# Kernel tuning notes

Measured on AMD Instinct MI355X. Metric: run time of the kernel, lower is better.

The kernel has to match this reference:

```python
import jax, jax.numpy as jnp
import numpy as np

N, D, E, K = 65536, 2048, 64, 8
EPS = 1e-5


def setup_inputs() -> dict:
    key = jax.random.key(0)
    kx, kw = jax.random.split(key)
    x = jax.random.normal(kx, (N, D), dtype=jnp.float32)
    # nn.Linear(input_size, num_experts, bias=False) weight: [E, D]
    W = jax.random.normal(kw, (E, D), dtype=jnp.float32) * (1.0 / np.sqrt(D))
    return {"x": x, "W": W}


def _l1_normalize(v):
    # torch F.normalize(p=1, dim=0): v / max(||v||_1, 1e-12)
    return v / jnp.maximum(jnp.sum(jnp.abs(v)), 1e-12)


def reference(x, W):
    # router logits: [N, E] in float32 (matches .float() in torch code)
    logits = (x @ W.T).astype(jnp.float32)
    top_v, top_i = jax.lax.top_k(logits, K)            # [N, K]
    top_k_gates = jax.nn.softmax(top_v, axis=-1).astype(x.dtype)
    # training-branch aux loss (compute_aux_loss)
    probs = jax.nn.softmax(logits, axis=-1)            # [N, E]
    rows = jnp.arange(logits.shape[0])[:, None]
    dense_gates = jnp.zeros_like(probs, dtype=top_k_gates.dtype).at[rows, top_i].set(top_k_gates)
    probs_sum = probs.sum(0)                           # [E]
    freq = (dense_gates > 0).astype(jnp.float32).sum(0)  # [E]
    # log(sum(exp(logits)) + eps)^2 summed, computed stably
    lse = jnp.logaddexp(jax.scipy.special.logsumexp(logits, axis=-1), jnp.log(EPS))
    zloss = jnp.sum(lse ** 2) / logits.shape[0]
    switchloss = E * jnp.sum(_l1_normalize(probs_sum) * _l1_normalize(freq))
    loss = switchloss + 0.1 * zloss
    return top_i, top_k_gates, loss
```

## Files before the change

### kernel.cpp

```cpp
#include <hip/hip_runtime.h>
#include <math.h>

#define NROWS 65536
#define DDIM 2048
#define NEXP 64
#define TOPK 8

constexpr int NSTEP = 64;
constexpr float THR = 3e-4f;
constexpr int WFRAG_STEP = 4096;
constexpr int CAP = 16384;

typedef short bf16x8 __attribute__((ext_vector_type(8)));
typedef float f32x4 __attribute__((ext_vector_type(4)));

__device__ inline unsigned short bfround(float f) {
    union { float f; unsigned u; } v; v.f = f;
    unsigned r = (v.u + 0x7fffu + ((v.u >> 16) & 1u)) >> 16;
    return (unsigned short)r;
}
__device__ inline float bf2f(unsigned short h) {
    union { unsigned u; float f; } v; v.u = ((unsigned)h) << 16;
    return v.f;
}
__device__ inline void cvt8(const float4& A, const float4& B, bf16x8& h, bf16x8& l) {
    float f[8] = {A.x, A.y, A.z, A.w, B.x, B.y, B.z, B.w};
#pragma unroll
    for (int j = 0; j < 8; ++j) {
        unsigned short hh = bfround(f[j]);
        h[j] = (short)hh;
        l[j] = (short)bfround(f[j] - bf2f(hh));
    }
}

__global__ __launch_bounds__(256)
void prep_kernel(const float* __restrict__ W, short* __restrict__ wfrag)
{
    const int t = blockIdx.x;
    const int tid = threadIdx.x;
    const int ct = tid >> 6, lane = tid & 63;
    const int e = ct * 16 + (lane & 15);
    const int k = t * 32 + (lane >> 4) * 8;
    const float* wp = W + (size_t)e * DDIM + k;
    float4 a = *reinterpret_cast<const float4*>(wp);
    float4 b = *reinterpret_cast<const float4*>(wp + 4);
    bf16x8 h, l;
    cvt8(a, b, h, l);
    short* base = wfrag + (size_t)t * WFRAG_STEP;
    *reinterpret_cast<bf16x8*>(base + (ct * 64 + lane) * 8) = h;
    *reinterpret_cast<bf16x8*>(base + 2048 + (ct * 64 + lane) * 8) = l;
}

__global__ __launch_bounds__(256, 2)
void gemm_kernel(const float* __restrict__ x, const short* __restrict__ wfrag,
                 float* __restrict__ logits)
{
    __shared__ __align__(16) short Bfrag[2][2][4][64][8];

    const int tid = threadIdx.x;
    const int w = tid >> 6;
    const int lane = tid & 63;
    const int g = lane >> 4;
    const int c = lane & 15;
    const int row0 = blockIdx.x * 64 + w * 16;
    const float* xr = x + (size_t)(row0 + c) * DDIM + g * 8;

    const int se = tid >> 2, skg = tid & 3;
    const int sct = se >> 4;
    const int slane = (se & 15) + (skg << 4);
    const int soff = (sct * 64 + slane) * 8;

    auto stageB = [&](int t, int buf) {
        const short* src = wfrag + (size_t)t * WFRAG_STEP + soff;
        *reinterpret_cast<bf16x8*>(&Bfrag[buf][0][sct][slane][0]) =
            *reinterpret_cast<const bf16x8*>(src);
        *reinterpret_cast<bf16x8*>(&Bfrag[buf][1][sct][slane][0]) =
            *reinterpret_cast<const bf16x8*>(src + 2048);
    };

    f32x4 acc[4];
#pragma unroll
    for (int ct = 0; ct < 4; ++ct) acc[ct] = (f32x4){0.f, 0.f, 0.f, 0.f};

    float4 xa0 = *reinterpret_cast<const float4*>(xr);
    float4 xa1 = *reinterpret_cast<const float4*>(xr + 4);
    float4 xb0, xb1;
    stageB(0, 0);
    __syncthreads();

    for (int t = 0; t < NSTEP; ++t) {
        const int buf = t & 1;
        const int kn = (t + 1) * 32;
        if (t + 1 < NSTEP) {
            xb0 = *reinterpret_cast<const float4*>(xr + kn);
            xb1 = *reinterpret_cast<const float4*>(xr + kn + 4);
            stageB(t + 1, buf ^ 1);
        }
        bf16x8 ah, al;
        cvt8(xa0, xa1, ah, al);
#pragma unroll
        for (int ct = 0; ct < 4; ++ct) {
            bf16x8 bh = *reinterpret_cast<const bf16x8*>(&Bfrag[buf][0][ct][lane][0]);
            bf16x8 bl = *reinterpret_cast<const bf16x8*>(&Bfrag[buf][1][ct][lane][0]);
            acc[ct] = __builtin_amdgcn_mfma_f32_16x16x32_bf16(ah, bh, acc[ct], 0, 0, 0);
            acc[ct] = __builtin_amdgcn_mfma_f32_16x16x32_bf16(ah, bl, acc[ct], 0, 0, 0);
            acc[ct] = __builtin_amdgcn_mfma_f32_16x16x32_bf16(al, bh, acc[ct], 0, 0, 0);
        }
        xa0 = xb0; xa1 = xb1;
        __syncthreads();
    }

#pragma unroll
    for (int ct = 0; ct < 4; ++ct)
#pragma unroll
        for (int reg = 0; reg < 4; ++reg)
            logits[(size_t)(row0 + g * 4 + reg) * NEXP + ct * 16 + c] = acc[ct][reg];
}

__global__ __launch_bounds__(256, 2)
void epilogue_kernel(const float* __restrict__ logits,
                     float* __restrict__ out_idx, float* __restrict__ out_gate,
                     float* __restrict__ g_psum, float* __restrict__ g_freq,
                     float* __restrict__ g_zsum, int* __restrict__ g_cnt,
                     int* __restrict__ g_rows)
{
    __shared__ float psum_s[NEXP];
    __shared__ float fcnt_s[NEXP];
    __shared__ float zsq_s;
    const int tid = threadIdx.x;
    const int w = tid >> 6;
    const int lane = tid & 63;
    const int g = lane >> 4;
    const int c = lane & 15;
    if (tid < NEXP) { psum_s[tid] = 0.f; fcnt_s[tid] = 0.f; }
    if (tid == 0) zsq_s = 0.f;
    __syncthreads();

    const int wi = blockIdx.x * 4 + w;
    float pcol[4] = {0.f, 0.f, 0.f, 0.f};
    float zacc = 0.f;

    for (int it = 0; it < 2; ++it) {
        const int row = wi * 8 + it * 4 + g;
        float4 Lv = *reinterpret_cast<const float4*>(&logits[(size_t)row * NEXP + c * 4]);
        float L[4] = {Lv.x, Lv.y, Lv.z, Lv.w};
        float ld[4] = {L[0], L[1], L[2], L[3]};

        float tv[9]; int ti[9];
#pragma unroll
        for (int p = 0; p < 9; ++p) {
            float bv = -3.4e38f; int bgi = 127;
#pragma unroll
            for (int j = 0; j < 4; ++j) {
                int e = c * 4 + j;
                if (ld[j] > bv) { bv = ld[j]; bgi = e; }
            }
#pragma unroll
            for (int m = 1; m < 16; m <<= 1) {
                float ov = __shfl_xor(bv, m, 16);
                int ogi = __shfl_xor(bgi, m, 16);
                if (ov > bv || (ov == bv && ogi < bgi)) { bv = ov; bgi = ogi; }
            }
            tv[p] = bv; ti[p] = bgi;
#pragma unroll
            for (int j = 0; j < 4; ++j)
                if (bgi == c * 4 + j) ld[j] = -3.4e38f;
        }

        const float m0 = tv[0];
        float pe[4], ps = 0.f;
#pragma unroll
        for (int j = 0; j < 4; ++j) { pe[j] = __expf(L[j] - m0); ps += pe[j]; }
        float s = ps;
#pragma unroll
        for (int m = 1; m < 16; m <<= 1) s += __shfl_xor(s, m, 16);
        const float inv_s = 1.f / s;
#pragma unroll
        for (int j = 0; j < 4; ++j) pcol[j] += pe[j] * inv_s;

        if (c == 0) {
            float lsef = m0 + __logf(s);
            const float lb = -11.512925464970229f;
            float mx = fmaxf(lsef, lb), mn = fminf(lsef, lb);
            float z = mx + log1pf(__expf(mn - mx));
            zacc += z * z;
        }

        float mg = 3.4e38f;
#pragma unroll
        for (int p = 0; p < 8; ++p) mg = fminf(mg, tv[p] - tv[p + 1]);
        const bool flagged = (mg < THR);
        const size_t base = (size_t)row * TOPK;

        float gs = 0.f;
#pragma unroll
        for (int p = 0; p < 8; ++p) gs += __expf(tv[p] - m0);
        if (c < 8) {
            float mytv = tv[0]; int myti = ti[0];
#pragma unroll
            for (int p = 1; p < 8; ++p)
                if (c == p) { mytv = tv[p]; myti = ti[p]; }
            out_idx[base + c] = (float)myti;
            out_gate[base + c] = __expf(mytv - m0) / gs;
            if (!flagged) atomicAdd(&fcnt_s[myti], 1.f);
        }
        if (flagged && c == 0) {
            int idx = atomicAdd(g_cnt, 1);
            if (idx < CAP) g_rows[idx] = row;
        }
    }

#pragma unroll
    for (int j = 0; j < 4; ++j) atomicAdd(&psum_s[c * 4 + j], pcol[j]);
    if (c == 0) atomicAdd(&zsq_s, zacc);
    __syncthreads();
    if (tid < NEXP) {
        atomicAdd(&g_psum[tid], psum_s[tid]);
        atomicAdd(&g_freq[tid], fcnt_s[tid]);
    }
    if (tid == 0) atomicAdd(g_zsum, zsq_s);
}

__global__ __launch_bounds__(256, 1)
void fixup_kernel(const float* __restrict__ x, const float* __restrict__ W,
                  const float* __restrict__ logits,
                  float* __restrict__ out_idx, float* __restrict__ out_gate,
                  float* __restrict__ g_freq,
                  const int* __restrict__ g_cnt, const int* __restrict__ g_rows)
{
    const int n = min(*g_cnt, CAP);
    const int lane = threadIdx.x & 63;
    const int wid = (blockIdx.x * blockDim.x + threadIdx.x) >> 6;
    const int nw = (gridDim.x * blockDim.x) >> 6;

    for (int i = wid; i < n; i += nw) {
        const int row = g_rows[i];
        const float lg = logits[(size_t)row * NEXP + lane];

        unsigned u = __float_as_uint(lg);
        unsigned ordb = (u & 0x80000000u) ? ~u : (u | 0x80000000u);
        unsigned long long key =
            ((unsigned long long)ordb << 32) | (unsigned)(63 - lane);
#pragma unroll
        for (int k = 2; k <= 64; k <<= 1) {
#pragma unroll
            for (int j = k >> 1; j > 0; j >>= 1) {
                unsigned long long other = __shfl_xor(key, j, 64);
                const bool keep_max = ((lane & j) == 0) == ((lane & k) == 0);
                const bool mine_bigger = key > other;
                key = (keep_max == mine_bigger) ? key : other;
            }
        }
        unsigned ou = (unsigned)(key >> 32);
        unsigned ub = (ou & 0x80000000u) ? (ou ^ 0x80000000u) : ~ou;
        const float val = __uint_as_float(ub);
        const float v9 = __shfl(val, 8, 64);

        const bool cand = (lg >= v9 - THR);
        unsigned long long cm = __ballot(cand);
        const float* xrw = x + (size_t)row * DDIM;
        float4 xv[8];
#pragma unroll
        for (int j = 0; j < 8; ++j)
            xv[j] = *reinterpret_cast<const float4*>(xrw + j * 256 + lane * 4);

        double myD = -HUGE_VAL;
        unsigned long long m2 = cm;
        while (m2) {
            const int e = (int)__ffsll((unsigned long long)m2) - 1;
            m2 &= (m2 - 1);
            const float* wrp = W + (size_t)e * DDIM;
            double p0 = 0.0, p1 = 0.0, p2 = 0.0, p3 = 0.0;
#pragma unroll
            for (int j = 0; j < 8; ++j) {
                float4 wv = *reinterpret_cast<const float4*>(wrp + j * 256 + lane * 4);
                p0 = fma((double)xv[j].x, (double)wv.x, p0);
                p1 = fma((double)xv[j].y, (double)wv.y, p1);
                p2 = fma((double)xv[j].z, (double)wv.z, p2);
                p3 = fma((double)xv[j].w, (double)wv.w, p3);
            }
            double sd = (p0 + p1) + (p2 + p3);
#pragma unroll
            for (int m = 1; m < 64; m <<= 1) sd += __shfl_xor(sd, m, 64);
            if (lane == e) myD = sd;
        }

        double v = cand ? myD : -HUGE_VAL;
        double tvd[8]; int ti8[8];
#pragma unroll
        for (int p = 0; p < 8; ++p) {
            double bv = v; int bgi = lane;
#pragma unroll
            for (int m = 1; m < 64; m <<= 1) {
                double ov = __shfl_xor(bv, m, 64);
                int ogi = __shfl_xor(bgi, m, 64);
                if (ov > bv || (ov == bv && ogi < bgi)) { bv = ov; bgi = ogi; }
            }
            tvd[p] = bv; ti8[p] = bgi;
            if (lane == bgi) v = -HUGE_VAL;
        }
        const double m0d = tvd[0];
        double gsum = 0.0, ge[8];
#pragma unroll
        for (int j = 0; j < 8; ++j) { ge[j] = exp(tvd[j] - m0d); gsum += ge[j]; }
        if (lane < 8) {
            double myge = ge[0]; int myti = ti8[0];
#pragma unroll
            for (int j = 1; j < 8; ++j)
                if (lane == j) { myge = ge[j]; myti = ti8[j]; }
            const size_t base = (size_t)row * TOPK;
            out_idx[base + lane] = (float)myti;
            out_gate[base + lane] = (float)(myge / gsum);
            atomicAdd(&g_freq[myti], 1.0f);
        }
    }
}

__global__ void finalize_kernel(const float* __restrict__ g_psum,
                                const float* __restrict__ g_freq,
                                const float* __restrict__ g_zsum,
                                float* __restrict__ out_loss)
{
    const int lane = threadIdx.x & 63;
    float p = g_psum[lane], f = g_freq[lane];
    float sp = p, sf = f;
#pragma unroll
    for (int m = 1; m < 64; m <<= 1) { sp += __shfl_xor(sp, m, 64); sf += __shfl_xor(sf, m, 64); }
    sp = fmaxf(sp, 1e-12f);
    sf = fmaxf(sf, 1e-12f);
    float term = (p / sp) * (f / sf);
#pragma unroll
    for (int m = 1; m < 64; m <<= 1) term += __shfl_xor(term, m, 64);
    if (lane == 0)
        out_loss[0] = (float)NEXP * term + 0.1f * (g_zsum[0] / (float)NROWS);
}

extern "C" void kernel_launch(void* const* d_in, const int* in_sizes, int n_in,
                              void* d_out, int out_size, void* d_ws, size_t ws_size,
                              hipStream_t stream)
{
    const float* x = (const float*)d_in[0];
    const float* W = (const float*)d_in[1];
    float* out = (float*)d_out;
    float* out_idx  = out;
    float* out_gate = out + (size_t)NROWS * TOPK;
    float* out_loss = out + (size_t)2 * NROWS * TOPK;

    float* acc    = (float*)d_ws;
    int*   cnt    = (int*)d_ws + 129;
    int*   rows   = (int*)d_ws + 130;
    float* logits = (float*)d_ws + 32768;
    short* wfrag  = (short*)((float*)d_ws + 32768 + (size_t)NROWS * NEXP);
    hipMemsetAsync(d_ws, 0, 132 * sizeof(float), stream);

    prep_kernel<<<NSTEP, 256, 0, stream>>>(W, wfrag);
    gemm_kernel<<<NROWS / 64, 256, 0, stream>>>(x, wfrag, logits);
    epilogue_kernel<<<2048, 256, 0, stream>>>(logits, out_idx, out_gate,
                                              acc, acc + NEXP, acc + 2 * NEXP,
                                              cnt, rows);
    fixup_kernel<<<512, 256, 0, stream>>>(x, W, logits, out_idx, out_gate,
                                          acc + NEXP, cnt, rows);
    finalize_kernel<<<1, 64, 0, stream>>>(acc, acc + NEXP, acc + 2 * NEXP, out_loss);
}
```

Before: 280.2 us.

## Fuse router top-k/softmax epilogue into GEMM kernel, store only flagged logits

Merges the epilogue into the GEMM kernel so top-k, softmax, z-loss and aux statistics are computed straight from MFMA accumulators in registers. The full 16 MB logits matrix is no longer written and re-read. Only rows flagged for near-ties have their logits saved to a compact buffer, which the fixup kernel now reads by index. This removes one launch and heavy memory traffic, at the cost of more register pressure in the GEMM kernel and a cross-lane broadcast of the slot index.

```diff
diff --git a/kernel.cpp b/kernel.cpp
--- a/kernel.cpp
+++ b/kernel.cpp
@@ -52,10 +52,16 @@
 }
 
 __global__ __launch_bounds__(256, 2)
-void gemm_kernel(const float* __restrict__ x, const short* __restrict__ wfrag,
-                 float* __restrict__ logits)
+void fused_kernel(const float* __restrict__ x, const short* __restrict__ wfrag,
+                  float* __restrict__ out_idx, float* __restrict__ out_gate,
+                  float* __restrict__ g_psum, float* __restrict__ g_freq,
+                  float* __restrict__ g_zsum, int* __restrict__ g_cnt,
+                  int* __restrict__ g_rows, float* __restrict__ g_logits)
 {
     __shared__ __align__(16) short Bfrag[2][2][4][64][8];
+    __shared__ float psum_s[NEXP];
+    __shared__ float fcnt_s[NEXP];
+    __shared__ float zsq_s;
 
     const int tid = threadIdx.x;
     const int w = tid >> 6;
@@ -65,6 +71,9 @@
     const int row0 = blockIdx.x * 64 + w * 16;
     const float* xr = x + (size_t)(row0 + c) * DDIM + g * 8;
 
+    if (tid < NEXP) { psum_s[tid] = 0.f; fcnt_s[tid] = 0.f; }
+    if (tid == 0) zsq_s = 0.f;
+
     const int se = tid >> 2, skg = tid & 3;
     const int sct = se >> 4;
     const int slane = (se & 15) + (skg << 4);
@@ -110,50 +119,24 @@
         __syncthreads();
     }
 
-#pragma unroll
-    for (int ct = 0; ct < 4; ++ct)
-#pragma unroll
-        for (int reg = 0; reg < 4; ++reg)
-            logits[(size_t)(row0 + g * 4 + reg) * NEXP + ct * 16 + c] = acc[ct][reg];
-}
-
-__global__ __launch_bounds__(256, 2)
-void epilogue_kernel(const float* __restrict__ logits,
-                     float* __restrict__ out_idx, float* __restrict__ out_gate,
-                     float* __restrict__ g_psum, float* __restrict__ g_freq,
-                     float* __restrict__ g_zsum, int* __restrict__ g_cnt,
-                     int* __restrict__ g_rows)
-{
-    __shared__ float psum_s[NEXP];
-    __shared__ float fcnt_s[NEXP];
-    __shared__ float zsq_s;
-    const int tid = threadIdx.x;
-    const int w = tid >> 6;
-    const int lane = tid & 63;
-    const int g = lane >> 4;
-    const int c = lane & 15;
-    if (tid < NEXP) { psum_s[tid] = 0.f; fcnt_s[tid] = 0.f; }
-    if (tid == 0) zsq_s = 0.f;
-    __syncthreads();
-
-    const int wi = blockIdx.x * 4 + w;
     float pcol[4] = {0.f, 0.f, 0.f, 0.f};
     float zacc = 0.f;
 
-    for (int it = 0; it < 2; ++it) {
-        const int row = wi * 8 + it * 4 + g;
-        float4 Lv = *reinterpret_cast<const float4*>(&logits[(size_t)row * NEXP + c * 4]);
-        float L[4] = {Lv.x, Lv.y, Lv.z, Lv.w};
-        float ld[4] = {L[0], L[1], L[2], L[3]};
+#pragma unroll
+    for (int reg = 0; reg < 4; ++reg) {
+        const int row = row0 + g * 4 + reg;
+        float ld[4];
+#pragma unroll
+        for (int ct = 0; ct < 4; ++ct) ld[ct] = acc[ct][reg];
 
         float tv[9]; int ti[9];
 #pragma unroll
         for (int p = 0; p < 9; ++p) {
             float bv = -3.4e38f; int bgi = 127;
 #pragma unroll
-            for (int j = 0; j < 4; ++j) {
-                int e = c * 4 + j;
-                if (ld[j] > bv) { bv = ld[j]; bgi = e; }
+            for (int ct = 0; ct < 4; ++ct) {
+                int e = ct * 16 + c;
+                if (ld[ct] > bv) { bv = ld[ct]; bgi = e; }
             }
 #pragma unroll
             for (int m = 1; m < 16; m <<= 1) {
@@ -163,20 +146,23 @@
             }
             tv[p] = bv; ti[p] = bgi;
 #pragma unroll
-            for (int j = 0; j < 4; ++j)
-                if (bgi == c * 4 + j) ld[j] = -3.4e38f;
+            for (int ct = 0; ct < 4; ++ct)
+                if (bgi == ct * 16 + c) ld[ct] = -3.4e38f;
         }
 
         const float m0 = tv[0];
         float pe[4], ps = 0.f;
 #pragma unroll
-        for (int j = 0; j < 4; ++j) { pe[j] = __expf(L[j] - m0); ps += pe[j]; }
+        for (int ct = 0; ct < 4; ++ct) {
+            pe[ct] = __expf(acc[ct][reg] - m0);
+            ps += pe[ct];
+        }
         float s = ps;
 #pragma unroll
         for (int m = 1; m < 16; m <<= 1) s += __shfl_xor(s, m, 16);
         const float inv_s = 1.f / s;
 #pragma unroll
-        for (int j = 0; j < 4; ++j) pcol[j] += pe[j] * inv_s;
+        for (int ct = 0; ct < 4; ++ct) pcol[ct] += pe[ct] * inv_s;
 
         if (c == 0) {
             float lsef = m0 + __logf(s);
@@ -204,14 +190,21 @@
             out_gate[base + c] = __expf(mytv - m0) / gs;
             if (!flagged) atomicAdd(&fcnt_s[myti], 1.f);
         }
-        if (flagged && c == 0) {
-            int idx = atomicAdd(g_cnt, 1);
-            if (idx < CAP) g_rows[idx] = row;
-        }
-    }
-
-#pragma unroll
-    for (int j = 0; j < 4; ++j) atomicAdd(&psum_s[c * 4 + j], pcol[j]);
+        if (flagged) {
+            int idx = 0;
+            if (c == 0) idx = atomicAdd(g_cnt, 1);
+            idx = __shfl(idx, (lane >> 4) << 4, 64);
+            if (idx < CAP) {
+                if (c == 0) g_rows[idx] = row;
+#pragma unroll
+                for (int ct = 0; ct < 4; ++ct)
+                    g_logits[(size_t)idx * NEXP + ct * 16 + c] = acc[ct][reg];
+            }
+        }
+    }
+
+#pragma unroll
+    for (int ct = 0; ct < 4; ++ct) atomicAdd(&psum_s[ct * 16 + c], pcol[ct]);
     if (c == 0) atomicAdd(&zsq_s, zacc);
     __syncthreads();
     if (tid < NEXP) {
@@ -223,10 +216,10 @@
 
 __global__ __launch_bounds__(256, 1)
 void fixup_kernel(const float* __restrict__ x, const float* __restrict__ W,
-                  const float* __restrict__ logits,
                   float* __restrict__ out_idx, float* __restrict__ out_gate,
                   float* __restrict__ g_freq,
-                  const int* __restrict__ g_cnt, const int* __restrict__ g_rows)
+                  const int* __restrict__ g_cnt, const int* __restrict__ g_rows,
+                  const float* __restrict__ g_logits)
 {
     const int n = min(*g_cnt, CAP);
     const int lane = threadIdx.x & 63;
@@ -235,7 +228,7 @@
 
     for (int i = wid; i < n; i += nw) {
         const int row = g_rows[i];
-        const float lg = logits[(size_t)row * NEXP + lane];
+        const float lg = g_logits[(size_t)i * NEXP + lane];
 
         unsigned u = __float_as_uint(lg);
         unsigned ordb = (u & 0x80000000u) ? ~u : (u | 0x80000000u);
@@ -346,19 +339,18 @@
     float* out_gate = out + (size_t)NROWS * TOPK;
     float* out_loss = out + (size_t)2 * NROWS * TOPK;
 
-    float* acc    = (float*)d_ws;
-    int*   cnt    = (int*)d_ws + 129;
-    int*   rows   = (int*)d_ws + 130;
-    float* logits = (float*)d_ws + 32768;
-    short* wfrag  = (short*)((float*)d_ws + 32768 + (size_t)NROWS * NEXP);
+    float* acc      = (float*)d_ws;
+    int*   cnt      = (int*)d_ws + 129;
+    int*   rows     = (int*)d_ws + 130;
+    float* g_logits = (float*)d_ws + 16896;
+    short* wfrag    = (short*)((float*)d_ws + 1065984);
     hipMemsetAsync(d_ws, 0, 132 * sizeof(float), stream);
 
     prep_kernel<<<NSTEP, 256, 0, stream>>>(W, wfrag);
-    gemm_kernel<<<NROWS / 64, 256, 0, stream>>>(x, wfrag, logits);
-    epilogue_kernel<<<2048, 256, 0, stream>>>(logits, out_idx, out_gate,
-                                              acc, acc + NEXP, acc + 2 * NEXP,
-                                              cnt, rows);
-    fixup_kernel<<<512, 256, 0, stream>>>(x, W, logits, out_idx, out_gate,
-                                          acc + NEXP, cnt, rows);
+    fused_kernel<<<NROWS / 64, 256, 0, stream>>>(
+        x, wfrag, out_idx, out_gate, acc, acc + NEXP, acc + 2 * NEXP,
+        cnt, rows, g_logits);
+    fixup_kernel<<<512, 256, 0, stream>>>(x, W, out_idx, out_gate, acc + NEXP,
+                                          cnt, rows, g_logits);
     finalize_kernel<<<1, 64, 0, stream>>>(acc, acc + NEXP, acc + 2 * NEXP, out_loss);
 }
```

New measurement: 244.2 us. 1.15x faster.
